# Kernel tuning notes

Measured on AMD Instinct MI355X. Metric: run time of the kernel, lower is better.

Reference implementation:

```python
import jax, jax.numpy as jnp
import numpy as np

H = 128; W = 128; HW = H * W
B = 4          # batch_size
D = 256        # feat_dim
HEADS = 8
HD = D // HEADS
S = 256        # num_slots_total
POS = 512      # num_pos_samples
NEG = 256      # num_neg_samples
NS = POS + NEG # num_samples
LN_EPS = 1e-5


def _layer_norm(x, axis=-1, eps=LN_EPS):
    mean = jnp.mean(x, axis=axis, keepdims=True)
    var = jnp.mean(jnp.square(x - mean), axis=axis, keepdims=True)
    return (x - mean) * jax.lax.rsqrt(var + eps)


def setup_inputs() -> dict:
    key = jax.random.key(0)
    ks = jax.random.split(key, 8)
    slots = jax.random.normal(ks[0], (1, S, D), jnp.float32)
    features = jax.random.normal(ks[1], (HW, B, D), jnp.float32)
    pos_encodings = jax.random.normal(ks[2], (HW, B, D), jnp.float32)
    curio_maps = jax.random.uniform(ks[3], (S, H, W), jnp.float32)
    batch_idx = jax.random.randint(ks[4], (S,), 0, B)
    scale = 1.0 / np.sqrt(D)
    in_proj_weight = jax.random.normal(ks[5], (3 * D, D), jnp.float32) * scale
    in_proj_bias = jnp.zeros((3 * D,), jnp.float32)
    out_proj_w = jax.random.normal(ks[6], (D, D), jnp.float32) * scale
    out_proj_b = jnp.zeros((D,), jnp.float32)
    ln_w = jnp.ones((D,), jnp.float32)
    ln_b = jnp.zeros((D,), jnp.float32)
    return {
        'slots': slots, 'features': features, 'pos_encodings': pos_encodings,
        'curio_maps': curio_maps, 'batch_idx': batch_idx,
        'in_proj_weight': in_proj_weight, 'in_proj_bias': in_proj_bias,
        'out_proj_w': out_proj_w, 'out_proj_b': out_proj_b,
        'ln_w': ln_w, 'ln_b': ln_b, 'max_mask_entries': 100,
    }


def reference(slots, features, pos_encodings, curio_maps, batch_idx,
              in_proj_weight, in_proj_bias, out_proj_w, out_proj_b,
              ln_w, ln_b, max_mask_entries):
    ns_total = slots.shape[1]
    # ---- sample(): curiosity-guided top-k sampling -------------------------
    flat = curio_maps.reshape(ns_total, -1)                 # [S, H*W]
    sorted_idx = jnp.argsort(-flat, axis=1)                 # descending
    pos_idx = sorted_idx[:, :POS]
    neg_pool = sorted_idx[:, POS:flat.shape[1] - max_mask_entries]
    # deterministic stand-in for random.sample over the negative pool
    neg_idx = neg_pool[:, :NEG]
    feat_idx = jnp.concatenate([pos_idx, neg_idx], axis=1).T  # [NS, S]

    # ---- update_slots(): gather + projected multi-head cross-attention -----
    bi = batch_idx[None, :]                                 # [1, S]
    f = features[feat_idx, bi, :]                           # [NS, S, D]
    p = pos_encodings[feat_idx, bi, :]                      # [NS, S, D]
    keys = f + p
    values = f[:POS]                                        # [POS, S, D]

    Wq, Wk, Wv = in_proj_weight[:D], in_proj_weight[D:2 * D], in_proj_weight[2 * D:]
    bq, bk, bv = in_proj_bias[:D], in_proj_bias[D:2 * D], in_proj_bias[2 * D:]
    scaling = float(HD) ** -0.5
    q = (jnp.einsum('bsd,ed->bse', slots, Wq) + bq) * scaling   # [1, S, D]
    k = jnp.einsum('nsd,ed->nse', keys, Wk) + bk                # [NS, S, D]
    v = jnp.einsum('nsd,ed->nse', values, Wv) + bv              # [POS, S, D]

    q = q.reshape(ns_total * HEADS, 1, HD)                      # [S*h, 1, hd]
    k = k.reshape(NS, ns_total * HEADS, HD).transpose(1, 0, 2)  # [S*h, NS, hd]
    v = v.reshape(POS, ns_total * HEADS, HD).transpose(1, 0, 2) # [S*h, POS, hd]

    aff = jnp.einsum('nqd,nkd->nqk', q, k)                      # [S*h, 1, NS]
    attn = jax.nn.softmax(aff[:, :, :POS], axis=-1)
    out = jnp.einsum('nqk,nkd->nqd', attn, v)                   # [S*h, 1, hd]
    out = out.reshape(1, ns_total, D)
    out = jnp.einsum('bsd,ed->bse', out, out_proj_w) + out_proj_b

    slots_new = slots + out
    slots_new = _layer_norm(slots_new, axis=-1) * ln_w + ln_b   # [1, S, D]

    # normalized slot-feature affinities (head-averaged, per-slot layernorm)
    aff2 = aff.reshape(ns_total, HEADS, NS).transpose(2, 0, 1)  # [NS, S, h]
    aff2 = jnp.mean(aff2, axis=-1)                              # [NS, S]
    norm_aff = _layer_norm(aff2.T, axis=-1).T                   # [NS, S]
    norm_aff = jax.lax.stop_gradient(norm_aff)
    return slots_new, norm_aff
```

## Files before the change

kernel.cpp:

```cpp
#include <hip/hip_runtime.h>
#include <math.h>

#define NSLOT 256
#define HWN   16384
#define D_    256
#define BB    4
#define NSEL  768
#define NPOS  512
#define NHEAD 8

typedef __attribute__((ext_vector_type(8))) short short8v;
typedef __attribute__((ext_vector_type(4))) float float4v;

#define GLD16(g, l)                                                        \
  __builtin_amdgcn_global_load_lds(                                        \
      (__attribute__((address_space(1))) void*)(g),                        \
      (__attribute__((address_space(3))) void*)(l), 16, 0, 0)

#define BFLO(u) __uint_as_float((u) << 16)
#define BFHI(u) __uint_as_float((u) & 0xffff0000u)

__device__ __forceinline__ unsigned short f2bf(float x) {
  unsigned u = __float_as_uint(x);
  unsigned r = u + 0x7fffu + ((u >> 16) & 1u);
  return (unsigned short)(r >> 16);
}
__device__ __forceinline__ unsigned int pk2(float a, float b) {
  return (unsigned)f2bf(a) | ((unsigned)f2bf(b) << 16);
}

union PrepSmem {
  struct {
    unsigned int hist[4096];
    unsigned int wsum[16];
    unsigned long long skey[2048];
    int sBstar;
    unsigned int sCount;
  } tk;
  struct {
    float srow[4][D_];
    float qrow[4][D_];
    float qkl[4][NHEAD][D_];
    float qsl[4][D_];
  } qp;
};

__global__ __launch_bounds__(1024) void prep_kernel(
    const float* __restrict__ curio, int* __restrict__ feat_sel,
    const float* __restrict__ slots, const float* __restrict__ ipw,
    const float* __restrict__ ipb, float* __restrict__ qbk_g,
    unsigned short* __restrict__ qkb16,
    const float* __restrict__ fsrc, const float* __restrict__ psrc,
    unsigned short* __restrict__ kpf) {
  __shared__ PrepSmem sm;
  int B = blockIdx.x;
  int t = threadIdx.x;

  if (B < 256) {
    int s = B;
    int wave = t >> 6, lane = t & 63;
    const float* row = curio + (size_t)s * HWN;

    for (int i = t; i < 4096; i += 1024) sm.tk.hist[i] = 0;
    if (t == 0) sm.tk.sCount = 0;
    __syncthreads();
    for (int j = t; j < HWN; j += 1024) {
      unsigned int bits = __float_as_uint(row[j]);
      atomicAdd(&sm.tk.hist[bits >> 18], 1u);
    }
    __syncthreads();
    unsigned int cs = sm.tk.hist[t * 4] + sm.tk.hist[t * 4 + 1] +
                      sm.tk.hist[t * 4 + 2] + sm.tk.hist[t * 4 + 3];
    unsigned int v = cs;
#pragma unroll
    for (int off = 1; off < 64; off <<= 1) {
      unsigned int u = __shfl_down(v, off, 64);
      if (lane + off < 64) v += u;
    }
    if (lane == 0) sm.tk.wsum[wave] = v;
    __syncthreads();
    unsigned int above = 0;
    for (int w2 = wave + 1; w2 < 16; w2++) above += sm.tk.wsum[w2];
    unsigned int sufAfter = above + (v - cs);
    if (sufAfter < NSEL && sufAfter + cs >= NSEL) {
      unsigned int local = sufAfter;
      for (int b2 = t * 4 + 3; b2 >= t * 4; b2--) {
        unsigned int c = sm.tk.hist[b2];
        if (local + c >= NSEL) { sm.tk.sBstar = b2; break; }
        local += c;
      }
    }
    __syncthreads();
    int bstar = sm.tk.sBstar;
    for (int j = t; j < HWN; j += 1024) {
      unsigned int bits = __float_as_uint(row[j]);
      if ((int)(bits >> 18) >= bstar) {
        unsigned int pos = atomicAdd(&sm.tk.sCount, 1u);
        if (pos < 2048)
          sm.tk.skey[pos] = ((unsigned long long)bits << 14) |
                            (unsigned long long)(16383 - j);
      }
    }
    __syncthreads();
    unsigned int M = sm.tk.sCount;
    int SZ = (M <= 1024) ? 1024 : 2048;
    for (int i = t; i < SZ; i += 1024) if (i >= (int)M) sm.tk.skey[i] = 0ull;
    for (int k = 2; k <= SZ; k <<= 1) {
      for (int j2 = k >> 1; j2 > 0; j2 >>= 1) {
        __syncthreads();
        for (int i = t; i < SZ; i += 1024) {
          int l = i ^ j2;
          if (l > i) {
            unsigned long long a = sm.tk.skey[i], b2 = sm.tk.skey[l];
            bool dir = ((i & k) == 0);
            if ((a < b2) == dir) { sm.tk.skey[i] = b2; sm.tk.skey[l] = a; }
          }
        }
      }
    }
    __syncthreads();
    for (int r = t; r < NSEL; r += 1024)
      feat_sel[s * NSEL + r] = 16383 - (int)(sm.tk.skey[r] & 16383ull);
  } else if (B < 320) {
    int sub = t >> 8, tt = t & 255;
    int s = (B - 256) * 4 + sub;
    float* srow = sm.qp.srow[sub];
    float* qrow = sm.qp.qrow[sub];
    float* qsl = sm.qp.qsl[sub];
    srow[tt] = slots[s * D_ + tt];
    __syncthreads();
    {
      const float* wq = ipw + (size_t)tt * D_;
      float acc = ipb[tt];
      for (int d = 0; d < D_; d++) acc += srow[d] * wq[d];
      qrow[tt] = acc * 0.17677669529663689f;
    }
    __syncthreads();
    float qsum = 0.f;
    for (int h = 0; h < NHEAD; h++) {
      const float* wkbase = ipw + (size_t)(D_ + h * 32) * D_ + tt;
      float a = 0.f;
      for (int e = 0; e < 32; e++) a += qrow[h * 32 + e] * wkbase[(size_t)e * D_];
      sm.qp.qkl[sub][h][tt] = a;
      qsum += a;
    }
    qsl[tt] = qsum;
    if (tt < NHEAD) {
      float a = 0.f;
      for (int e = 0; e < 32; e++) a += qrow[tt * 32 + e] * ipb[D_ + tt * 32 + e];
      qbk_g[s * NHEAD + tt] = a;
    }
    __syncthreads();
    for (int i = 0; i < 16; i++) {
      int e = tt * 16 + i;
      int kc = e >> 9, l = (e >> 3) & 63, j = e & 7;
      int cc = l & 15, k = kc * 32 + ((l >> 4) & 3) * 8 + j;
      float v = (cc < NHEAD) ? sm.qp.qkl[sub][cc][k] : ((cc == NHEAD) ? qsl[k] : 0.f);
      qkb16[(size_t)s * 4096 + e] = f2bf(v);
    }
  } else {
    int stride = 512 * 1024;
    for (int u = (B - 320) * 1024 + t; u < HWN * BB * 32; u += stride) {
      int row = u >> 5, b2 = u & 31;
      int c8 = b2 << 3;
      const float4* f4 = (const float4*)(fsrc + (size_t)row * D_ + c8);
      const float4* p4 = (const float4*)(psrc + (size_t)row * D_ + c8);
      float4 a0 = f4[0], a1 = f4[1], b0 = p4[0], b1 = p4[1];
      uint4 kp, ff;
      kp.x = pk2(a0.x + b0.x, a0.y + b0.y);
      kp.y = pk2(a0.z + b0.z, a0.w + b0.w);
      kp.z = pk2(a1.x + b1.x, a1.y + b1.y);
      kp.w = pk2(a1.z + b1.z, a1.w + b1.w);
      ff.x = pk2(a0.x, a0.y); ff.y = pk2(a0.z, a0.w);
      ff.z = pk2(a1.x, a1.y); ff.w = pk2(a1.z, a1.w);
      int sig = row & 7;
      *(uint4*)(kpf + (size_t)row * 512 + ((b2 ^ sig) << 3)) = kp;
      *(uint4*)(kpf + (size_t)row * 512 + 256 + (c8)) = ff;
    }
  }
}

__global__ __launch_bounds__(256, 3) void aff_pv_mfma_kernel(
    const unsigned short* __restrict__ kpf,
    const unsigned short* __restrict__ qkb16,
    const int* __restrict__ batch_idx, const int* __restrict__ feat_sel,
    const float* __restrict__ qbk_g,
    float* __restrict__ fbar_part,
    float* __restrict__ expsum_part,
    float* __restrict__ stat_part,
    float* __restrict__ aff2_g) {
  __shared__ unsigned short kplds[4][4096];
  __shared__ unsigned short qkb[4096];
  __shared__ float wlds[4][16][17];
  __shared__ float fbar[NHEAD][D_];
  __shared__ float a2buf[384];
  __shared__ int   sfsel[384];
  __shared__ float esums[4][NHEAD];
  __shared__ float sstat[4][2];
  __shared__ float qbkmean_s;

  int b = blockIdx.x, s = b >> 1, half = b & 1;
  int t = threadIdx.x, w = t >> 6, lane = t & 63;
  int bi = batch_idx[s];
  int col = lane & 15, quad = lane >> 4;

  {
    const uint4* src = (const uint4*)(qkb16 + (size_t)s * 4096);
    ((uint4*)qkb)[t] = src[t];
    ((uint4*)qkb)[t + 256] = src[t + 256];
  }
  for (int i = t; i < 384; i += 256) sfsel[i] = feat_sel[s * NSEL + half + 2 * i];
  for (int i = t; i < NHEAD * D_; i += 256) ((float*)fbar)[i] = 0.f;
  if (t == 0) {
    float m = 0.f;
    for (int h = 0; h < NHEAD; h++) m += qbk_g[s * NHEAD + h];
    qbkmean_s = m * 0.125f;
  }
  __syncthreads();

  unsigned short* kslot = &kplds[w][0];
  float acc[NHEAD][4];
#pragma unroll
  for (int h = 0; h < NHEAD; h++)
#pragma unroll
    for (int c = 0; c < 4; c++) acc[h][c] = 0.f;
  float esum_acc = 0.f;

  auto ISSUE_KP = [&](int L) {
#pragma unroll
    for (int p = 0; p < 8; p++) {
      int r0 = sfsel[L + 2 * p], r1 = sfsel[L + 2 * p + 1];
      unsigned ridx = (unsigned)((lane < 32 ? r0 : r1) * BB + bi);
      const unsigned short* src = kpf + (size_t)ridx * 512 + (lane & 31) * 8;
      GLD16(src, kslot + p * 512);
    }
  };

  ISSUE_KP(w * 64);
#pragma unroll 1
  for (int i = 0; i < 6; i++) {
    int L = (i < 4) ? (w * 64 + i * 16) : (256 + w * 32 + (i - 4) * 16);
    asm volatile("s_waitcnt vmcnt(0)" ::: "memory");
    bool pos = (i < 4);
    uint2 fu[16];
    if (pos) {
#pragma unroll
      for (int r = 0; r < 16; r++)
        fu[r] = *(const uint2*)(kpf + (size_t)((unsigned)sfsel[L + r] * BB + bi) * 512 +
                                256 + lane * 4);
    }
    unsigned sig = ((unsigned)sfsel[L + col] * BB + bi) & 7u;
    short8v afr[8];
#pragma unroll
    for (int kc = 0; kc < 8; kc++) {
      unsigned blk = ((unsigned)(kc * 4 + quad)) ^ sig;
      afr[kc] = *(const short8v*)(kslot + col * 256 + blk * 8);
    }
    asm volatile("s_waitcnt lgkmcnt(0)" ::: "memory");
    __builtin_amdgcn_sched_barrier(0);
    if (i < 5) {
      int Ln = (i < 3) ? (w * 64 + (i + 1) * 16) : (256 + w * 32 + (i - 3) * 16);
      ISSUE_KP(Ln);
    }
    float4v c = {0.f, 0.f, 0.f, 0.f};
#pragma unroll
    for (int kc = 0; kc < 8; kc++) {
      short8v bfr = *(const short8v*)&qkb[(kc * 64 + lane) * 8];
      c = __builtin_amdgcn_mfma_f32_16x16x32_bf16(afr[kc], bfr, c, 0, 0, 0);
    }
    if (pos) {
      if (col < NHEAD) {
        float e0 = __expf(c[0]), e1 = __expf(c[1]), e2 = __expf(c[2]), e3 = __expf(c[3]);
        esum_acc += e0 + e1 + e2 + e3;
        wlds[w][quad * 4 + 0][col] = e0;
        wlds[w][quad * 4 + 1][col] = e1;
        wlds[w][quad * 4 + 2][col] = e2;
        wlds[w][quad * 4 + 3][col] = e3;
      } else if (col == NHEAD) {
        float qm = qbkmean_s;
#pragma unroll
        for (int j = 0; j < 4; j++) a2buf[L + quad * 4 + j] = c[j] * 0.125f + qm;
      }
      asm volatile("s_waitcnt lgkmcnt(0)" ::: "memory");
      __builtin_amdgcn_sched_barrier(0);
#pragma unroll
      for (int r = 0; r < 16; r++) {
        const float4 w0 = *(const float4*)&wlds[w][r][0];
        const float4 w1 = *(const float4*)&wlds[w][r][4];
        float f0 = BFLO(fu[r].x), f1 = BFHI(fu[r].x), f2 = BFLO(fu[r].y), f3 = BFHI(fu[r].y);
        acc[0][0] += w0.x * f0; acc[0][1] += w0.x * f1; acc[0][2] += w0.x * f2; acc[0][3] += w0.x * f3;
        acc[1][0] += w0.y * f0; acc[1][1] += w0.y * f1; acc[1][2] += w0.y * f2; acc[1][3] += w0.y * f3;
        acc[2][0] += w0.z * f0; acc[2][1] += w0.z * f1; acc[2][2] += w0.z * f2; acc[2][3] += w0.z * f3;
        acc[3][0] += w0.w * f0; acc[3][1] += w0.w * f1; acc[3][2] += w0.w * f2; acc[3][3] += w0.w * f3;
        acc[4][0] += w1.x * f0; acc[4][1] += w1.x * f1; acc[4][2] += w1.x * f2; acc[4][3] += w1.x * f3;
        acc[5][0] += w1.y * f0; acc[5][1] += w1.y * f1; acc[5][2] += w1.y * f2; acc[5][3] += w1.y * f3;
        acc[6][0] += w1.z * f0; acc[6][1] += w1.z * f1; acc[6][2] += w1.z * f2; acc[6][3] += w1.z * f3;
        acc[7][0] += w1.w * f0; acc[7][1] += w1.w * f1; acc[7][2] += w1.w * f2; acc[7][3] += w1.w * f3;
      }
    } else {
      if (col == NHEAD) {
        float qm = qbkmean_s;
#pragma unroll
        for (int j = 0; j < 4; j++) a2buf[L + quad * 4 + j] = c[j] * 0.125f + qm;
      }
    }
  }

  esum_acc += __shfl_xor(esum_acc, 16, 64);
  esum_acc += __shfl_xor(esum_acc, 32, 64);
  if (lane < NHEAD) esums[w][lane] = esum_acc;
#pragma unroll
  for (int h = 0; h < NHEAD; h++) {
    atomicAdd(&fbar[h][lane * 4 + 0], acc[h][0]);
    atomicAdd(&fbar[h][lane * 4 + 1], acc[h][1]);
    atomicAdd(&fbar[h][lane * 4 + 2], acc[h][2]);
    atomicAdd(&fbar[h][lane * 4 + 3], acc[h][3]);
  }
  __syncthreads();

  {
    float v1 = a2buf[t];
    float v2 = (t < 128) ? a2buf[256 + t] : 0.f;
    float ls = v1 + v2, lq = v1 * v1 + v2 * v2;
#pragma unroll
    for (int off = 32; off >= 1; off >>= 1) { ls += __shfl_xor(ls, off, 64); lq += __shfl_xor(lq, off, 64); }
    if (lane == 0) { sstat[w][0] = ls; sstat[w][1] = lq; }
  }
  __syncthreads();
  if (t < NHEAD) {
    expsum_part[b * NHEAD + t] = esums[0][t] + esums[1][t] + esums[2][t] + esums[3][t];
  } else if (t == NHEAD) {
    stat_part[b * 2 + 0] = sstat[0][0] + sstat[1][0] + sstat[2][0] + sstat[3][0];
    stat_part[b * 2 + 1] = sstat[0][1] + sstat[1][1] + sstat[2][1] + sstat[3][1];
  }
  aff2_g[s * NSEL + half + 2 * t] = a2buf[t];
  if (t < 128) aff2_g[s * NSEL + half + 2 * (256 + t)] = a2buf[256 + t];
  ((float4*)(fbar_part + (size_t)b * 2048))[t] = ((float4*)fbar)[t];
  ((float4*)(fbar_part + (size_t)b * 2048))[t + 256] = ((float4*)fbar)[t + 256];
}

__global__ __launch_bounds__(1024) void finish_kernel(
    const float* __restrict__ slots,
    const float* __restrict__ expsum_part, const float* __restrict__ stat_part,
    const float* __restrict__ aff2_g, const float* __restrict__ fbar_part,
    const float* __restrict__ ipw, const float* __restrict__ ipb,
    const float* __restrict__ wout, const float* __restrict__ bout,
    const float* __restrict__ lnw, const float* __restrict__ lnb,
    float* __restrict__ slots_new, float* __restrict__ norm_aff) {
  __shared__ float fbar[NHEAD][D_];
  __shared__ float srow[D_];
  __shared__ float outv[D_];
  __shared__ float pq[1024];
  __shared__ float redS[4], redQ[4];
  int s = blockIdx.x, t = threadIdx.x, wave = t >> 6, lane = t & 63;

  float st0 = stat_part[s * 4 + 0] + stat_part[s * 4 + 2];
  float st1 = stat_part[s * 4 + 1] + stat_part[s * 4 + 3];
  float mean_a = st0 * (1.0f / NSEL);
  float var_a = st1 * (1.0f / NSEL) - mean_a * mean_a;
  float rstd_a = rsqrtf(var_a + 1e-5f);
  if (t < NSEL) norm_aff[(size_t)t * NSLOT + s] = (aff2_g[s * NSEL + t] - mean_a) * rstd_a;

  if (t < 512) {
    int h = t >> 6;
    float inv = 1.0f / (expsum_part[s * 16 + h] + expsum_part[s * 16 + 8 + h]);
    const float4 a = ((const float4*)(fbar_part + (size_t)s * 4096))[t];
    const float4 c = ((const float4*)(fbar_part + (size_t)s * 4096 + 2048))[t];
    float4 r;
    r.x = (a.x + c.x) * inv; r.y = (a.y + c.y) * inv;
    r.z = (a.z + c.z) * inv; r.w = (a.w + c.w) * inv;
    ((float4*)fbar)[t] = r;
  }
  if (t < 64) ((float4*)srow)[t] = ((const float4*)(slots + (size_t)s * D_))[t];
  __syncthreads();

  {
    int o = t >> 2, part = t & 3, h = o >> 5;
    const float4* wv = (const float4*)(ipw + (size_t)(2 * D_ + o) * D_ + part * 64);
    float a = 0.f;
#pragma unroll
    for (int i = 0; i < 16; i++) {
      float4 w = wv[i];
      int d = part * 64 + i * 4;
      a += fbar[h][d] * w.x + fbar[h][d + 1] * w.y + fbar[h][d + 2] * w.z + fbar[h][d + 3] * w.w;
    }
    pq[t] = a;
  }
  __syncthreads();
  if (t < D_)
    outv[t] = pq[t * 4] + pq[t * 4 + 1] + pq[t * 4 + 2] + pq[t * 4 + 3] + ipb[2 * D_ + t];
  __syncthreads();

  {
    int o = t >> 2, part = t & 3;
    const float4* w4 = (const float4*)(wout + (size_t)o * D_ + part * 64);
    float a = 0.f;
#pragma unroll
    for (int i = 0; i < 16; i++) {
      float4 w = w4[i];
      int d = part * 64 + i * 4;
      a += outv[d] * w.x + outv[d + 1] * w.y + outv[d + 2] * w.z + outv[d + 3] * w.w;
    }
    pq[t] = a;
  }
  __syncthreads();
  float v = 0.f;
  if (t < D_) {
    v = srow[t] + pq[t * 4] + pq[t * 4 + 1] + pq[t * 4 + 2] + pq[t * 4 + 3] + bout[t];
    float ls = v, lq = v * v;
#pragma unroll
    for (int off = 32; off >= 1; off >>= 1) { ls += __shfl_xor(ls, off, 64); lq += __shfl_xor(lq, off, 64); }
    if (lane == 0) { redS[wave] = ls; redQ[wave] = lq; }
  }
  __syncthreads();
  if (t < D_) {
    float tots = redS[0] + redS[1] + redS[2] + redS[3];
    float totq = redQ[0] + redQ[1] + redQ[2] + redQ[3];
    float mean = tots * (1.0f / D_);
    float var = totq * (1.0f / D_) - mean * mean;
    float rstd = rsqrtf(var + 1e-5f);
    slots_new[s * D_ + t] = (v - mean) * rstd * lnw[t] + lnb[t];
  }
}

extern "C" void kernel_launch(void* const* d_in, const int* in_sizes, int n_in,
                              void* d_out, int out_size, void* d_ws, size_t ws_size,
                              hipStream_t stream) {
  const float* slots    = (const float*)d_in[0];
  const float* features = (const float*)d_in[1];
  const float* posenc   = (const float*)d_in[2];
  const float* curio    = (const float*)d_in[3];
  const int*   batch_idx= (const int*)d_in[4];
  const float* ipw      = (const float*)d_in[5];
  const float* ipb      = (const float*)d_in[6];
  const float* wout     = (const float*)d_in[7];
  const float* bout     = (const float*)d_in[8];
  const float* lnw      = (const float*)d_in[9];
  const float* lnb      = (const float*)d_in[10];

  char* ws = (char*)d_ws;
  size_t off = 0;
  int*   feat_sel    = (int*)(ws + off);   off += 256 * 768 * 4;
  float* qbk_g       = (float*)(ws + off); off += 256 * 8 * 4;
  unsigned short* qkb16 = (unsigned short*)(ws + off); off += 256 * 4096 * 2;
  float* fbar_part   = (float*)(ws + off); off += 256 * 2 * 8 * 256 * 4;
  float* expsum_part = (float*)(ws + off); off += 256 * 2 * 8 * 4;
  float* stat_part   = (float*)(ws + off); off += 256 * 2 * 2 * 4;
  float* aff2_g      = (float*)(ws + off); off += 256 * 768 * 4;
  size_t kpf_off = (off + 1023) & ~(size_t)1023;
  unsigned short* kpf = (unsigned short*)(ws + kpf_off);

  float* out_f = (float*)d_out;

  prep_kernel<<<832, 1024, 0, stream>>>(curio, feat_sel, slots, ipw, ipb,
                                        qbk_g, qkb16, features, posenc, kpf);
  aff_pv_mfma_kernel<<<NSLOT * 2, 256, 0, stream>>>(kpf, qkb16, batch_idx, feat_sel,
                                                    qbk_g, fbar_part, expsum_part,
                                                    stat_part, aff2_g);
  finish_kernel<<<NSLOT, 1024, 0, stream>>>(slots, expsum_part, stat_part, aff2_g,
                                            fbar_part, ipw, ipb, wout, bout, lnw, lnb,
                                            out_f, out_f + 65536);
}
```

Measured before the change: 144.1 us.

## Replace block bitonic sort with wave-level segment sorts and merge-rank

Candidate compaction in the top-k selection now uses one wave-level ballot and atomic per wave instead of a per-thread shared atomic. The full 1024/2048-element block bitonic sort, with a barrier per stage, is replaced by 64-element bitonic sorts done in registers with cross-lane shuffles. Each key's final rank then comes from binary searches into the other sorted segments. This removes most block-wide barriers in the sort. The trade-off is that candidates are capped at 1280 instead of 2048, which could drop valid entries when the threshold bucket is large.

Result: faster. 137.5 us (-4.6%).

```diff
diff --git a/kernel.cpp b/kernel.cpp
--- a/kernel.cpp
+++ b/kernel.cpp
@@ -8,6 +8,7 @@
 #define NSEL  768
 #define NPOS  512
 #define NHEAD 8
+#define SEGS  20
 
 typedef __attribute__((ext_vector_type(8))) short short8v;
 typedef __attribute__((ext_vector_type(4))) float float4v;
@@ -33,7 +34,7 @@
   struct {
     unsigned int hist[4096];
     unsigned int wsum[16];
-    unsigned long long skey[2048];
+    unsigned long long skey[SEGS * 64];
     int sBstar;
     unsigned int sCount;
   } tk;
@@ -94,33 +95,57 @@
     int bstar = sm.tk.sBstar;
     for (int j = t; j < HWN; j += 1024) {
       unsigned int bits = __float_as_uint(row[j]);
-      if ((int)(bits >> 18) >= bstar) {
-        unsigned int pos = atomicAdd(&sm.tk.sCount, 1u);
-        if (pos < 2048)
+      bool cand = ((int)(bits >> 18) >= bstar);
+      unsigned long long mask = __ballot(cand);
+      unsigned int base = 0;
+      int lcnt = __popcll(mask);
+      if (lane == 0 && lcnt) base = atomicAdd(&sm.tk.sCount, (unsigned)lcnt);
+      base = __shfl(base, 0, 64);
+      if (cand) {
+        unsigned pos = base + __popcll(mask & ((1ull << lane) - 1ull));
+        if (pos < SEGS * 64)
           sm.tk.skey[pos] = ((unsigned long long)bits << 14) |
                             (unsigned long long)(16383 - j);
       }
     }
     __syncthreads();
     unsigned int M = sm.tk.sCount;
-    int SZ = (M <= 1024) ? 1024 : 2048;
-    for (int i = t; i < SZ; i += 1024) if (i >= (int)M) sm.tk.skey[i] = 0ull;
-    for (int k = 2; k <= SZ; k <<= 1) {
-      for (int j2 = k >> 1; j2 > 0; j2 >>= 1) {
-        __syncthreads();
-        for (int i = t; i < SZ; i += 1024) {
-          int l = i ^ j2;
-          if (l > i) {
-            unsigned long long a = sm.tk.skey[i], b2 = sm.tk.skey[l];
-            bool dir = ((i & k) == 0);
-            if ((a < b2) == dir) { sm.tk.skey[i] = b2; sm.tk.skey[l] = a; }
-          }
+    if (M > SEGS * 64) M = SEGS * 64;
+    for (int i = t; i < SEGS * 64; i += 1024) if (i >= (int)M) sm.tk.skey[i] = 0ull;
+    __syncthreads();
+    for (int seg = wave; seg < SEGS; seg += 16) {
+      unsigned long long kv = sm.tk.skey[seg * 64 + lane];
+#pragma unroll
+      for (int k = 2; k <= 64; k <<= 1) {
+#pragma unroll
+        for (int j2 = k >> 1; j2 > 0; j2 >>= 1) {
+          unsigned long long o = __shfl_xor(kv, j2, 64);
+          bool lower = ((lane & j2) == 0);
+          bool descblk = ((lane & k) == 0);
+          bool wantmax = (descblk == lower);
+          kv = (wantmax == (kv >= o)) ? kv : o;
         }
       }
-    }
-    __syncthreads();
-    for (int r = t; r < NSEL; r += 1024)
-      feat_sel[s * NSEL + r] = 16383 - (int)(sm.tk.skey[r] & 16383ull);
+      sm.tk.skey[seg * 64 + lane] = kv;
+    }
+    __syncthreads();
+    for (int e = t; e < SEGS * 64; e += 1024) {
+      unsigned long long key = sm.tk.skey[e];
+      if (key == 0ull) continue;
+      int seg = e >> 6;
+      int rank = e & 63;
+      for (int g = 0; g < SEGS; g++) {
+        if (g == seg) continue;
+        const unsigned long long* sp = &sm.tk.skey[g * 64];
+        int lo = 0, hi = 64;
+        while (lo < hi) {
+          int mid = (lo + hi) >> 1;
+          if (sp[mid] > key) lo = mid + 1; else hi = mid;
+        }
+        rank += lo;
+      }
+      if (rank < NSEL) feat_sel[s * NSEL + rank] = 16383 - (int)(key & 16383ull);
+    }
   } else if (B < 320) {
     int sub = t >> 8, tt = t & 255;
     int s = (B - 256) * 4 + sub;
@@ -175,7 +200,7 @@
       ff.z = pk2(a1.x, a1.y); ff.w = pk2(a1.z, a1.w);
       int sig = row & 7;
       *(uint4*)(kpf + (size_t)row * 512 + ((b2 ^ sig) << 3)) = kp;
-      *(uint4*)(kpf + (size_t)row * 512 + 256 + (c8)) = ff;
+      *(uint4*)(kpf + (size_t)row * 512 + 256 + c8) = ff;
     }
   }
 }
```
